# Optimization experiments

Measured on AMD Instinct MI355X. Metric: run time of the kernel, lower is better.

Reference implementation:

```python
import jax, jax.numpy as jnp
import numpy as np

N = 20000
E = 320000
IN_DIM = 128
HID = 64
HEADS = 8
OUT_DIM = 128
NEG_SLOPE = 0.2  # PyG GATConv default leaky_relu slope


def _glorot(key, shape):
    fan_in = shape[0] if len(shape) > 1 else shape[-1]
    return jax.random.normal(key, shape, dtype=jnp.float32) / jnp.sqrt(jnp.float32(fan_in))


def setup_inputs() -> dict:
    key = jax.random.key(0)
    ks = jax.random.split(key, 16)
    x = jax.random.normal(ks[0], (N, IN_DIM), dtype=jnp.float32)
    edge_index = jax.random.randint(ks[1], (2, E), 0, N, dtype=jnp.int32)
    HC = HEADS * HID
    return {
        "x": x,
        "edge_index": edge_index,
        # layer 1: in -> heads*hid (concat)
        "W1": _glorot(ks[2], (IN_DIM, HC)),
        "a_src1": _glorot(ks[3], (HEADS, HID)),
        "a_dst1": _glorot(ks[4], (HEADS, HID)),
        "b1": jnp.zeros((HC,), jnp.float32),
        # layer 2: heads*hid -> heads*hid (concat)
        "W2": _glorot(ks[5], (HC, HC)),
        "a_src2": _glorot(ks[6], (HEADS, HID)),
        "a_dst2": _glorot(ks[7], (HEADS, HID)),
        "b2": jnp.zeros((HC,), jnp.float32),
        # layer 3: heads*hid -> out, heads=1, concat=False
        "W3": _glorot(ks[8], (HC, OUT_DIM)),
        "a_src3": _glorot(ks[9], (1, OUT_DIM)),
        "a_dst3": _glorot(ks[10], (1, OUT_DIM)),
        "b3": jnp.zeros((OUT_DIM,), jnp.float32),
    }


def _gat_layer(x, src, dst, W, a_src, a_dst, b, heads, concat):
    # x: [N, F_in] -> h: [N, H, C]
    n = x.shape[0]
    h = (x @ W).reshape(n, heads, -1)
    # per-node attention half-logits: [N, H]
    al_src = jnp.sum(h * a_src[None], axis=-1)
    al_dst = jnp.sum(h * a_dst[None], axis=-1)
    # per-edge logits with leaky relu: [E, H]
    e = jax.nn.leaky_relu(al_src[src] + al_dst[dst], NEG_SLOPE)
    # segment softmax over incoming edges of each dst node
    emax = jax.ops.segment_max(e, dst, num_segments=n)
    ex = jnp.exp(e - emax[dst])
    den = jax.ops.segment_sum(ex, dst, num_segments=n)
    alpha = ex / (den[dst] + 1e-16)
    # weighted scatter-aggregate of source features: [E, H, C] -> [N, H, C]
    out = jax.ops.segment_sum(h[src] * alpha[:, :, None], dst, num_segments=n)
    out = out.reshape(n, -1) if concat else out.mean(axis=1)
    return out + b


def reference(x, edge_index, W1, a_src1, a_dst1, b1, W2, a_src2, a_dst2, b2,
              W3, a_src3, a_dst3, b3):
    # PyG GATConv adds self-loops by default
    loops = jnp.arange(N, dtype=edge_index.dtype)
    src = jnp.concatenate([edge_index[0], loops])
    dst = jnp.concatenate([edge_index[1], loops])
    # eval mode: dropout is identity
    h = _gat_layer(x, src, dst, W1, a_src1, a_dst1, b1, HEADS, True)
    h = jax.nn.elu(h)
    h = _gat_layer(h, src, dst, W2, a_src2, a_dst2, b2, HEADS, True)
    h = jax.nn.elu(h)
    out = _gat_layer(h, src, dst, W3, a_src3, a_dst3, b3, 1, False)
    return out
```

## Files before the change

kernel.cpp:

```cpp
#include <hip/hip_runtime.h>
#include <math.h>

#define NN 20000
#define EE 320000
#define ETOT 340000
#define NHEADS 8
#define HID 64
#define HCV 512
#define IND 128
#define OUTD 128
#define NEG_SLOPE 0.2f

typedef __attribute__((ext_vector_type(8))) _Float16 half8;
typedef __attribute__((ext_vector_type(4))) float floatx4;

__device__ __forceinline__ void cvt_one(const float* W, _Float16* T, int idx, int K, int N) {
    int k = idx / N, n = idx - k * N;
    T[(size_t)n * K + k] = (_Float16)W[idx];
}

#define S1 (IND * HCV)
#define S2 (HCV * HCV)
#define S3 (HCV * OUTD)
#define STOT (S1 + S2 + S3)
#define XTOT (NN * IND)
__global__ void prep_kernel(const float* __restrict__ W1, const float* __restrict__ W2,
                            const float* __restrict__ W3, const float* __restrict__ x,
                            _Float16* __restrict__ T1, _Float16* __restrict__ T2,
                            _Float16* __restrict__ T3, _Float16* __restrict__ xh,
                            int* __restrict__ cnt) {
    int idx = blockIdx.x * blockDim.x + threadIdx.x;
    if (idx < S1) cvt_one(W1, T1, idx, IND, HCV);
    else if (idx < S1 + S2) cvt_one(W2, T2, idx - S1, HCV, HCV);
    else if (idx < STOT) cvt_one(W3, T3, idx - S1 - S2, HCV, OUTD);
    else if (idx < STOT + NN) cnt[idx - STOT] = 0;
    else if (idx < STOT + NN + XTOT) {
        int j = idx - STOT - NN;
        xh[j] = (_Float16)x[j];
    }
}


__global__ void count_kernel(const int* __restrict__ ei, int* __restrict__ cnt) {
    int i = blockIdx.x * blockDim.x + threadIdx.x;
    if (i >= ETOT) return;
    int v = (i < EE) ? ei[EE + i] : (i - EE);
    atomicAdd(&cnt[v], 1);
}

#define SCH 20
__global__ __launch_bounds__(1024) void scan_kernel(const int* __restrict__ cnt,
                                                    int* __restrict__ row_ptr,
                                                    int* __restrict__ cursor) {
    __shared__ int wtot[16];
    __shared__ int woff[16];
    int t = threadIdx.x;
    int lane = t & 63;
    int wid = t >> 6;
    int base = t * SCH;
    int vals[SCH];
    int s = 0;
    #pragma unroll
    for (int i = 0; i < SCH; i++) {
        int idx = base + i;
        int v = (idx < NN) ? cnt[idx] : 0;
        vals[i] = v;
        s += v;
    }
    int incl = s;
    #pragma unroll
    for (int off = 1; off < 64; off <<= 1) {
        int u = __shfl_up(incl, off);
        if (lane >= off) incl += u;
    }
    int excl = incl - s;
    if (lane == 63) wtot[wid] = incl;
    __syncthreads();
    if (t == 0) {
        int run = 0;
        #pragma unroll
        for (int j = 0; j < 16; j++) { woff[j] = run; run += wtot[j]; }
        row_ptr[NN] = run;
    }
    __syncthreads();
    int run = woff[wid] + excl;
    #pragma unroll
    for (int i = 0; i < SCH; i++) {
        int idx = base + i;
        if (idx < NN) { row_ptr[idx] = run; cursor[idx] = run; run += vals[i]; }
    }
}

__global__ void fill_kernel(const int* __restrict__ ei, int* __restrict__ cursor,
                            int* __restrict__ csr_src) {
    int i = blockIdx.x * blockDim.x + threadIdx.x;
    if (i >= ETOT) return;
    int u, v;
    if (i < EE) { u = ei[i]; v = ei[EE + i]; }
    else        { u = i - EE; v = i - EE; }
    int pos = atomicAdd(&cursor[v], 1);
    csr_src[pos] = u;
}

#define LDK 40
__global__ __launch_bounds__(512) void gemm_al(const _Float16* __restrict__ A,
                                               const _Float16* __restrict__ Bt,
                                               _Float16* __restrict__ C16,
                                               const float* __restrict__ a_src,
                                               const float* __restrict__ a_dst,
                                               float* __restrict__ als2,
                                               float* __restrict__ ald2,
                                               int M, int K) {
    __shared__ _Float16 sA[128 * LDK];
    __shared__ _Float16 sB[128 * LDK];
    __shared__ float psum_s[4][128];
    __shared__ float psum_d[4][128];
    int tid = threadIdx.x;
    int lane = tid & 63;
    int wid = tid >> 6;
    int wv_m = wid >> 2;
    int wv_n = wid & 3;
    int m0 = blockIdx.x * 128, n0 = blockIdx.y * 128;
    int quad = lane >> 4;
    int l15 = lane & 15;
    int arow = tid >> 2;
    int ac4 = tid & 3;

    floatx4 acc[4][2] = {};

    for (int k0 = 0; k0 < K; k0 += 32) {
        {
            int gm = m0 + arow;
            int4 va;
            if (gm < M) va = *(const int4*)&A[(size_t)gm * K + k0 + ac4 * 8];
            else        va = make_int4(0, 0, 0, 0);
            *(int4*)&sA[arow * LDK + ac4 * 8] = va;
            int gn = n0 + arow;
            int4 vb = *(const int4*)&Bt[(size_t)gn * K + k0 + ac4 * 8];
            *(int4*)&sB[arow * LDK + ac4 * 8] = vb;
        }
        __syncthreads();
        half8 a[4], b[2];
        #pragma unroll
        for (int i = 0; i < 4; i++)
            a[i] = *(const half8*)&sA[(wv_m * 64 + i * 16 + l15) * LDK + quad * 8];
        #pragma unroll
        for (int j = 0; j < 2; j++)
            b[j] = *(const half8*)&sB[(wv_n * 32 + j * 16 + l15) * LDK + quad * 8];
        #pragma unroll
        for (int i = 0; i < 4; i++)
            #pragma unroll
            for (int j = 0; j < 2; j++)
                acc[i][j] = __builtin_amdgcn_mfma_f32_16x16x32_f16(a[i], b[j], acc[i][j], 0, 0, 0);
        __syncthreads();
    }
    #pragma unroll
    for (int i = 0; i < 4; i++) {
        #pragma unroll
        for (int r = 0; r < 4; r++) {
            int gm = m0 + wv_m * 64 + i * 16 + quad * 4 + r;
            if (gm < M) {
                #pragma unroll
                for (int j = 0; j < 2; j++)
                    C16[(size_t)gm * HCV + n0 + wv_n * 32 + j * 16 + l15] = (_Float16)acc[i][j][r];
            }
        }
    }
    int h0 = n0 >> 6;
    int hh = h0 + (wv_n >> 1);
    float as_v[2], ad_v[2];
    #pragma unroll
    for (int j = 0; j < 2; j++) {
        int dim = (wv_n * 32 + j * 16 + l15) & 63;
        as_v[j] = a_src[hh * HID + dim];
        ad_v[j] = a_dst[hh * HID + dim];
    }
    #pragma unroll
    for (int i = 0; i < 4; i++) {
        #pragma unroll
        for (int r = 0; r < 4; r++) {
            float ps = acc[i][0][r] * as_v[0] + acc[i][1][r] * as_v[1];
            float pd = acc[i][0][r] * ad_v[0] + acc[i][1][r] * ad_v[1];
            #pragma unroll
            for (int off = 1; off <= 8; off <<= 1) {
                ps += __shfl_xor(ps, off);
                pd += __shfl_xor(pd, off);
            }
            if (l15 == 0) {
                int row = wv_m * 64 + i * 16 + quad * 4 + r;
                psum_s[wv_n][row] = ps;
                psum_d[wv_n][row] = pd;
            }
        }
    }
    __syncthreads();
    if (tid < 128) {
        int gm = m0 + tid;
        if (gm < M) {
            als2[(size_t)h0 * NN + gm]       = psum_s[0][tid] + psum_s[1][tid];
            als2[(size_t)(h0 + 1) * NN + gm] = psum_s[2][tid] + psum_s[3][tid];
            ald2[(size_t)h0 * NN + gm]       = psum_d[0][tid] + psum_d[1][tid];
            ald2[(size_t)(h0 + 1) * NN + gm] = psum_d[2][tid] + psum_d[3][tid];
        }
    }
}

__global__ __launch_bounds__(256) void gemm3(const _Float16* __restrict__ A,
                                             const _Float16* __restrict__ Bt,
                                             _Float16* __restrict__ C16,
                                             const float* __restrict__ a_src,
                                             const float* __restrict__ a_dst,
                                             float* __restrict__ als,
                                             float* __restrict__ ald,
                                             int M, int K) {
    __shared__ _Float16 sA[64 * LDK];
    __shared__ _Float16 sB[128 * LDK];
    __shared__ float psum_s[4][64];
    __shared__ float psum_d[4][64];
    int tid = threadIdx.x;
    int lane = tid & 63;
    int wv = tid >> 6;
    int m0 = blockIdx.x * 64;
    int quad = lane >> 4;
    int l15 = lane & 15;
    int arow = tid >> 2;
    int ac4 = tid & 3;

    floatx4 acc[4][2] = {};

    for (int k0 = 0; k0 < K; k0 += 32) {
        {
            int gm = m0 + arow;
            int4 va;
            if (gm < M && arow < 64) va = *(const int4*)&A[(size_t)gm * K + k0 + ac4 * 8];
            else                     va = make_int4(0, 0, 0, 0);
            if (arow < 64) *(int4*)&sA[arow * LDK + ac4 * 8] = va;
            #pragma unroll
            for (int r = 0; r < 2; r++) {
                int gn = arow + r * 64;
                int4 vb = *(const int4*)&Bt[(size_t)gn * K + k0 + ac4 * 8];
                *(int4*)&sB[(arow + r * 64) * LDK + ac4 * 8] = vb;
            }
        }
        __syncthreads();
        half8 a[4], b[2];
        #pragma unroll
        for (int i = 0; i < 4; i++)
            a[i] = *(const half8*)&sA[(i * 16 + l15) * LDK + quad * 8];
        #pragma unroll
        for (int j = 0; j < 2; j++)
            b[j] = *(const half8*)&sB[(wv * 32 + j * 16 + l15) * LDK + quad * 8];
        #pragma unroll
        for (int i = 0; i < 4; i++)
            #pragma unroll
            for (int j = 0; j < 2; j++)
                acc[i][j] = __builtin_amdgcn_mfma_f32_16x16x32_f16(a[i], b[j], acc[i][j], 0, 0, 0);
        __syncthreads();
    }
    #pragma unroll
    for (int i = 0; i < 4; i++) {
        #pragma unroll
        for (int r = 0; r < 4; r++) {
            int gm = m0 + i * 16 + quad * 4 + r;
            if (gm < M) {
                #pragma unroll
                for (int j = 0; j < 2; j++)
                    C16[(size_t)gm * OUTD + wv * 32 + j * 16 + l15] = (_Float16)acc[i][j][r];
            }
        }
    }
    float as_v[2], ad_v[2];
    #pragma unroll
    for (int j = 0; j < 2; j++) {
        as_v[j] = a_src[wv * 32 + j * 16 + l15];
        ad_v[j] = a_dst[wv * 32 + j * 16 + l15];
    }
    #pragma unroll
    for (int i = 0; i < 4; i++) {
        #pragma unroll
        for (int r = 0; r < 4; r++) {
            float ps = acc[i][0][r] * as_v[0] + acc[i][1][r] * as_v[1];
            float pd = acc[i][0][r] * ad_v[0] + acc[i][1][r] * ad_v[1];
            #pragma unroll
            for (int off = 1; off <= 8; off <<= 1) {
                ps += __shfl_xor(ps, off);
                pd += __shfl_xor(pd, off);
            }
            if (l15 == 0) {
                int row = i * 16 + quad * 4 + r;
                psum_s[wv][row] = ps;
                psum_d[wv][row] = pd;
            }
        }
    }
    __syncthreads();
    if (tid < 64) {
        int gm = m0 + tid;
        if (gm < M) {
            als[gm] = psum_s[0][tid] + psum_s[1][tid] + psum_s[2][tid] + psum_s[3][tid];
            ald[gm] = psum_d[0][tid] + psum_d[1][tid] + psum_d[2][tid] + psum_d[3][tid];
        }
    }
}

__global__ __launch_bounds__(256) void gather_kernel(const _Float16* __restrict__ h,
                                                     const int* __restrict__ row_ptr,
                                                     const int* __restrict__ csr_src,
                                                     const float* __restrict__ als2,
                                                     const float* __restrict__ ald2,
                                                     const float* __restrict__ bias,
                                                     _Float16* __restrict__ gout) {
    int tid = threadIdx.x;
    int lane = tid & 63;
    int wid = tid >> 6;
    int bid = blockIdx.x;
    int hd = bid & 7;
    int sub = lane >> 3;
    int dl = lane & 7;
    int v = (bid >> 3) * 32 + wid * 8 + sub;
    if (v >= NN) return;
    const float* asl = als2 + (size_t)hd * NN;
    float adst = ald2[(size_t)hd * NN + v];
    int s0 = row_ptr[v], s1 = row_ptr[v + 1];
    const _Float16* hh = h + hd * HID + dl * 8;
    float acc[8] = {};
    float l = 0.f;
    int j = s0;
    for (; j + 4 <= s1; j += 4) {
        int u[4]; float p[4]; half8 xv[4];
        #pragma unroll
        for (int e = 0; e < 4; e++) u[e] = csr_src[j + e];
        #pragma unroll
        for (int e = 0; e < 4; e++) xv[e] = *(const half8*)&hh[(size_t)u[e] * HCV];
        #pragma unroll
        for (int e = 0; e < 4; e++) {
            float t = asl[u[e]] + adst;
            t = (t > 0.f) ? t : NEG_SLOPE * t;
            p[e] = __expf(fminf(t, 80.f));
        }
        #pragma unroll
        for (int e = 0; e < 4; e++) {
            l += p[e];
            #pragma unroll
            for (int k = 0; k < 8; k++)
                acc[k] = fmaf(p[e], (float)xv[e][k], acc[k]);
        }
    }
    for (; j < s1; j++) {
        int u0 = csr_src[j];
        half8 x0 = *(const half8*)&hh[(size_t)u0 * HCV];
        float t0 = asl[u0] + adst;
        t0 = (t0 > 0.f) ? t0 : NEG_SLOPE * t0;
        float p0 = __expf(fminf(t0, 80.f));
        l += p0;
        #pragma unroll
        for (int k = 0; k < 8; k++)
            acc[k] = fmaf(p0, (float)x0[k], acc[k]);
    }
    float inv = 1.f / (l + 1e-16f);
    half8 hv;
    #pragma unroll
    for (int k = 0; k < 8; k++) {
        float o = fmaf(acc[k], inv, bias[hd * HID + dl * 8 + k]);
        o = (o > 0.f) ? o : (__expf(o) - 1.f);
        hv[k] = (_Float16)o;
    }
    half8* dst = (half8*)&gout[(size_t)v * HCV + hd * HID + dl * 8];
    __builtin_nontemporal_store(hv, dst);
}

__global__ __launch_bounds__(256) void gather3_kernel(const _Float16* __restrict__ h,
                                                      const int* __restrict__ row_ptr,
                                                      const int* __restrict__ csr_src,
                                                      const float* __restrict__ als,
                                                      const float* __restrict__ ald,
                                                      const float* __restrict__ bias,
                                                      float* __restrict__ out) {
    int tid = threadIdx.x;
    int lane = tid & 63;
    int wid = tid >> 6;
    int bid = blockIdx.x;
    int dh = bid & 1;
    int sub = lane >> 3;
    int dl = lane & 7;
    int v = (bid >> 1) * 32 + wid * 8 + sub;
    if (v >= NN) return;
    float adst = ald[v];
    int s0 = row_ptr[v], s1 = row_ptr[v + 1];
    const _Float16* hh = h + dh * 64 + dl * 8;
    float m = -INFINITY;
    for (int j = s0; j < s1; j++) {
        int u = csr_src[j];
        float t = als[u] + adst;
        t = (t > 0.f) ? t : NEG_SLOPE * t;
        m = fmaxf(m, t);
    }
    float acc[8] = {};
    float l = 0.f;
    int j = s0;
    for (; j + 2 <= s1; j += 2) {
        int u0 = csr_src[j], u1 = csr_src[j + 1];
        float t0 = als[u0] + adst;
        float t1 = als[u1] + adst;
        t0 = (t0 > 0.f) ? t0 : NEG_SLOPE * t0;
        t1 = (t1 > 0.f) ? t1 : NEG_SLOPE * t1;
        float p0 = __expf(t0 - m);
        float p1 = __expf(t1 - m);
        half8 x0 = *(const half8*)&hh[(size_t)u0 * OUTD];
        half8 x1 = *(const half8*)&hh[(size_t)u1 * OUTD];
        l += p0 + p1;
        #pragma unroll
        for (int k = 0; k < 8; k++) {
            acc[k] = fmaf(p0, (float)x0[k], acc[k]);
            acc[k] = fmaf(p1, (float)x1[k], acc[k]);
        }
    }
    if (j < s1) {
        int u0 = csr_src[j];
        float t0 = als[u0] + adst;
        t0 = (t0 > 0.f) ? t0 : NEG_SLOPE * t0;
        float p0 = __expf(t0 - m);
        half8 x0 = *(const half8*)&hh[(size_t)u0 * OUTD];
        l += p0;
        #pragma unroll
        for (int k = 0; k < 8; k++)
            acc[k] = fmaf(p0, (float)x0[k], acc[k]);
    }
    float inv = 1.f / (l + 1e-16f);
    float4 o0, o1;
    o0.x = fmaf(acc[0], inv, bias[dh * 64 + dl * 8 + 0]);
    o0.y = fmaf(acc[1], inv, bias[dh * 64 + dl * 8 + 1]);
    o0.z = fmaf(acc[2], inv, bias[dh * 64 + dl * 8 + 2]);
    o0.w = fmaf(acc[3], inv, bias[dh * 64 + dl * 8 + 3]);
    o1.x = fmaf(acc[4], inv, bias[dh * 64 + dl * 8 + 4]);
    o1.y = fmaf(acc[5], inv, bias[dh * 64 + dl * 8 + 5]);
    o1.z = fmaf(acc[6], inv, bias[dh * 64 + dl * 8 + 6]);
    o1.w = fmaf(acc[7], inv, bias[dh * 64 + dl * 8 + 7]);
    size_t base = (size_t)v * OUTD + dh * 64 + dl * 8;
    *(float4*)&out[base] = o0;
    *(float4*)&out[base + 4] = o1;
}


extern "C" void kernel_launch(void* const* d_in, const int* in_sizes, int n_in,
                              void* d_out, int out_size, void* d_ws, size_t ws_size,
                              hipStream_t stream) {
    const float* x     = (const float*)d_in[0];
    const int*   ei    = (const int*)d_in[1];
    const float* W1    = (const float*)d_in[2];
    const float* as1   = (const float*)d_in[3];
    const float* ad1   = (const float*)d_in[4];
    const float* b1    = (const float*)d_in[5];
    const float* W2    = (const float*)d_in[6];
    const float* as2   = (const float*)d_in[7];
    const float* ad2   = (const float*)d_in[8];
    const float* b2    = (const float*)d_in[9];
    const float* W3    = (const float*)d_in[10];
    const float* as3   = (const float*)d_in[11];
    const float* ad3   = (const float*)d_in[12];
    const float* b3    = (const float*)d_in[13];
    float* out = (float*)d_out;

    size_t off = 0;
    auto carve = [&](size_t bytes) {
        void* p = (char*)d_ws + off;
        off += (bytes + 255) & ~(size_t)255;
        return p;
    };
    int* row_ptr   = (int*)carve((NN + 1) * sizeof(int));
    int* cursor    = (int*)carve(NN * sizeof(int));
    int* csr_src   = (int*)carve(ETOT * sizeof(int));
    _Float16* xh   = (_Float16*)carve((size_t)NN * IND * sizeof(_Float16));
    _Float16* h1   = (_Float16*)carve((size_t)NN * HCV * sizeof(_Float16));
    _Float16* gact = (_Float16*)carve((size_t)NN * HCV * sizeof(_Float16));
    _Float16* hf16 = (_Float16*)carve((size_t)NN * HCV * sizeof(_Float16));
    _Float16* h3   = (_Float16*)carve((size_t)NN * OUTD * sizeof(_Float16));
    float* als     = (float*)carve((size_t)NN * NHEADS * sizeof(float));
    float* ald     = (float*)carve((size_t)NN * NHEADS * sizeof(float));
    _Float16* W1T  = (_Float16*)carve((size_t)S1 * sizeof(_Float16));
    _Float16* W2T  = (_Float16*)carve((size_t)S2 * sizeof(_Float16));
    _Float16* W3T  = (_Float16*)carve((size_t)S3 * sizeof(_Float16));
    _Float16* gact2 = h1;
    (void)ws_size; (void)n_in; (void)in_sizes; (void)out_size;

    dim3 blk(256);

    int prep_n = STOT + NN + XTOT;
    prep_kernel<<<(prep_n + 255) / 256, blk, 0, stream>>>(W1, W2, W3, x,
        W1T, W2T, W3T, xh, cursor);

    count_kernel<<<(ETOT + 255) / 256, blk, 0, stream>>>(ei, cursor);
    scan_kernel<<<1, 1024, 0, stream>>>(cursor, row_ptr, cursor);
    fill_kernel<<<(ETOT + 255) / 256, blk, 0, stream>>>(ei, cursor, csr_src);

    int mt64 = (NN + 63) / 64;
    int mt128 = (NN + 127) / 128;
    int nb = (NN + 31) / 32;

    gemm_al<<<dim3(mt128, HCV / 128), dim3(512), 0, stream>>>(xh, W1T, h1, as1, ad1, als, ald, NN, IND);
    gather_kernel<<<dim3(nb * 8), blk, 0, stream>>>(h1, row_ptr, csr_src, als, ald, b1, gact);

    gemm_al<<<dim3(mt128, HCV / 128), dim3(512), 0, stream>>>(gact, W2T, hf16, as2, ad2, als, ald, NN, HCV);
    gather_kernel<<<dim3(nb * 8), blk, 0, stream>>>(hf16, row_ptr, csr_src, als, ald, b2, gact2);

    gemm3<<<dim3(mt64, 1), blk, 0, stream>>>(gact2, W3T, h3, as3, ad3, als, ald, NN, HCV);
    gather3_kernel<<<dim3(nb * 2), blk, 0, stream>>>(h3, row_ptr, csr_src, als, ald, b3, out);
}
```

Measured before the change: 312.5 us.

## Split edge lists across two lane groups, tile weight transpose, use exp2

The gather kernels now split each destination node's edge range between two 8-lane groups and combine the partial sums and normalisers with a lane shuffle. This doubles the parallelism per node and shortens the serial edge loop. The layer-3 max pass is spread over 16 lanes with a shuffle reduction. The prep kernel replaces the strided per-element weight transpose with shared-memory 32x32 tiles and a float4 vectorised x conversion. The attention vectors are pre-scaled by log2(e) so exp2f can replace expf. The costs are more blocks, cross-lane shuffles, and half the lanes idle during the output epilogue.

```diff
diff --git a/kernel.cpp b/kernel.cpp
--- a/kernel.cpp
+++ b/kernel.cpp
@@ -10,33 +10,63 @@
 #define IND 128
 #define OUTD 128
 #define NEG_SLOPE 0.2f
+#define LOG2E 1.4426950408889634f
 
 typedef __attribute__((ext_vector_type(8))) _Float16 half8;
+typedef __attribute__((ext_vector_type(4))) _Float16 half4;
 typedef __attribute__((ext_vector_type(4))) float floatx4;
-
-__device__ __forceinline__ void cvt_one(const float* W, _Float16* T, int idx, int K, int N) {
-    int k = idx / N, n = idx - k * N;
-    T[(size_t)n * K + k] = (_Float16)W[idx];
-}
 
 #define S1 (IND * HCV)
 #define S2 (HCV * HCV)
 #define S3 (HCV * OUTD)
-#define STOT (S1 + S2 + S3)
 #define XTOT (NN * IND)
-__global__ void prep_kernel(const float* __restrict__ W1, const float* __restrict__ W2,
-                            const float* __restrict__ W3, const float* __restrict__ x,
-                            _Float16* __restrict__ T1, _Float16* __restrict__ T2,
-                            _Float16* __restrict__ T3, _Float16* __restrict__ xh,
-                            int* __restrict__ cnt) {
-    int idx = blockIdx.x * blockDim.x + threadIdx.x;
-    if (idx < S1) cvt_one(W1, T1, idx, IND, HCV);
-    else if (idx < S1 + S2) cvt_one(W2, T2, idx - S1, HCV, HCV);
-    else if (idx < STOT) cvt_one(W3, T3, idx - S1 - S2, HCV, OUTD);
-    else if (idx < STOT + NN) cnt[idx - STOT] = 0;
-    else if (idx < STOT + NN + XTOT) {
-        int j = idx - STOT - NN;
-        xh[j] = (_Float16)x[j];
+
+#define NT1 64
+#define NT2 320
+#define NT_TOT 384
+#define XB 2500
+__global__ __launch_bounds__(256) void prep_kernel(const float* __restrict__ W1,
+                                                   const float* __restrict__ W2,
+                                                   const float* __restrict__ W3,
+                                                   const float* __restrict__ x,
+                                                   _Float16* __restrict__ T1,
+                                                   _Float16* __restrict__ T2,
+                                                   _Float16* __restrict__ T3,
+                                                   _Float16* __restrict__ xh,
+                                                   int* __restrict__ cnt) {
+    int b = blockIdx.x;
+    int tid = threadIdx.x;
+    if (b < NT_TOT) {
+        __shared__ _Float16 tile[32][34];
+        const float* W; _Float16* T; int K, N, tb;
+        if (b < NT1)      { W = W1; T = T1; K = IND; N = HCV;  tb = b; }
+        else if (b < NT2) { W = W2; T = T2; K = HCV; N = HCV;  tb = b - NT1; }
+        else              { W = W3; T = T3; K = HCV; N = OUTD; tb = b - NT2; }
+        int ntn = N >> 5;
+        int k0 = (tb / ntn) * 32, n0 = (tb % ntn) * 32;
+        int tx = tid & 31, ty0 = tid >> 5;
+        #pragma unroll
+        for (int i = 0; i < 4; i++) {
+            int ty = ty0 + 8 * i;
+            tile[ty][tx] = (_Float16)W[(size_t)(k0 + ty) * N + n0 + tx];
+        }
+        __syncthreads();
+        #pragma unroll
+        for (int i = 0; i < 4; i++) {
+            int ty = ty0 + 8 * i;
+            T[(size_t)(n0 + ty) * K + k0 + tx] = tile[tx][ty];
+        }
+    } else if (b < NT_TOT + XB) {
+        int idx = (b - NT_TOT) * 256 + tid;
+        int j = idx * 4;
+        float4 v = *(const float4*)&x[j];
+        half4 o;
+        o[0] = (_Float16)v.x; o[1] = (_Float16)v.y;
+        o[2] = (_Float16)v.z; o[3] = (_Float16)v.w;
+        *(half4*)&xh[j] = o;
+    } else {
+        int idx = (b - NT_TOT - XB) * 256 + tid;
+        if (idx < NN) cnt[idx] = 0;
     }
 }
 
@@ -172,8 +202,8 @@
     #pragma unroll
     for (int j = 0; j < 2; j++) {
         int dim = (wv_n * 32 + j * 16 + l15) & 63;
-        as_v[j] = a_src[hh * HID + dim];
-        ad_v[j] = a_dst[hh * HID + dim];
+        as_v[j] = a_src[hh * HID + dim] * LOG2E;
+        ad_v[j] = a_dst[hh * HID + dim] * LOG2E;
     }
     #pragma unroll
     for (int i = 0; i < 4; i++) {
@@ -272,8 +302,8 @@
     float as_v[2], ad_v[2];
     #pragma unroll
     for (int j = 0; j < 2; j++) {
-        as_v[j] = a_src[wv * 32 + j * 16 + l15];
-        ad_v[j] = a_dst[wv * 32 + j * 16 + l15];
+        as_v[j] = a_src[wv * 32 + j * 16 + l15] * LOG2E;
+        ad_v[j] = a_dst[wv * 32 + j * 16 + l15] * LOG2E;
     }
     #pragma unroll
     for (int i = 0; i < 4; i++) {
@@ -315,18 +345,22 @@
     int wid = tid >> 6;
     int bid = blockIdx.x;
     int hd = bid & 7;
-    int sub = lane >> 3;
     int dl = lane & 7;
-    int v = (bid >> 3) * 32 + wid * 8 + sub;
+    int es = (lane >> 3) & 1;
+    int sub = lane >> 4;
+    int v = (bid >> 3) * 16 + wid * 4 + sub;
     if (v >= NN) return;
     const float* asl = als2 + (size_t)hd * NN;
     float adst = ald2[(size_t)hd * NN + v];
     int s0 = row_ptr[v], s1 = row_ptr[v + 1];
+    int mid = (s0 + s1 + 1) >> 1;
+    int jb = es ? mid : s0;
+    int je = es ? s1 : mid;
     const _Float16* hh = h + hd * HID + dl * 8;
     float acc[8] = {};
     float l = 0.f;
-    int j = s0;
-    for (; j + 4 <= s1; j += 4) {
+    int j = jb;
+    for (; j + 4 <= je; j += 4) {
         int u[4]; float p[4]; half8 xv[4];
         #pragma unroll
         for (int e = 0; e < 4; e++) u[e] = csr_src[j + e];
@@ -336,7 +370,7 @@
         for (int e = 0; e < 4; e++) {
             float t = asl[u[e]] + adst;
             t = (t > 0.f) ? t : NEG_SLOPE * t;
-            p[e] = __expf(fminf(t, 80.f));
+            p[e] = exp2f(fminf(t, 115.f));
         }
         #pragma unroll
         for (int e = 0; e < 4; e++) {
@@ -346,27 +380,33 @@
                 acc[k] = fmaf(p[e], (float)xv[e][k], acc[k]);
         }
     }
-    for (; j < s1; j++) {
+    for (; j < je; j++) {
         int u0 = csr_src[j];
         half8 x0 = *(const half8*)&hh[(size_t)u0 * HCV];
         float t0 = asl[u0] + adst;
         t0 = (t0 > 0.f) ? t0 : NEG_SLOPE * t0;
-        float p0 = __expf(fminf(t0, 80.f));
+        float p0 = exp2f(fminf(t0, 115.f));
         l += p0;
         #pragma unroll
         for (int k = 0; k < 8; k++)
             acc[k] = fmaf(p0, (float)x0[k], acc[k]);
     }
-    float inv = 1.f / (l + 1e-16f);
-    half8 hv;
-    #pragma unroll
-    for (int k = 0; k < 8; k++) {
-        float o = fmaf(acc[k], inv, bias[hd * HID + dl * 8 + k]);
-        o = (o > 0.f) ? o : (__expf(o) - 1.f);
-        hv[k] = (_Float16)o;
-    }
-    half8* dst = (half8*)&gout[(size_t)v * HCV + hd * HID + dl * 8];
-    __builtin_nontemporal_store(hv, dst);
+    l += __shfl_xor(l, 8);
+    #pragma unroll
+    for (int k = 0; k < 8; k++)
+        acc[k] += __shfl_xor(acc[k], 8);
+    if (es == 0) {
+        float inv = 1.f / (l + 1e-16f);
+        half8 hv;
+        #pragma unroll
+        for (int k = 0; k < 8; k++) {
+            float o = fmaf(acc[k], inv, bias[hd * HID + dl * 8 + k]);
+            o = (o > 0.f) ? o : (__expf(o) - 1.f);
+            hv[k] = (_Float16)o;
+        }
+        half8* dst = (half8*)&gout[(size_t)v * HCV + hd * HID + dl * 8];
+        __builtin_nontemporal_store(hv, dst);
+    }
 }
 
 __global__ __launch_bounds__(256) void gather3_kernel(const _Float16* __restrict__ h,
@@ -381,31 +421,39 @@
     int wid = tid >> 6;
     int bid = blockIdx.x;
     int dh = bid & 1;
-    int sub = lane >> 3;
     int dl = lane & 7;
-    int v = (bid >> 1) * 32 + wid * 8 + sub;
+    int es = (lane >> 3) & 1;
+    int sub = lane >> 4;
+    int l16 = lane & 15;
+    int v = (bid >> 1) * 16 + wid * 4 + sub;
     if (v >= NN) return;
     float adst = ald[v];
     int s0 = row_ptr[v], s1 = row_ptr[v + 1];
-    const _Float16* hh = h + dh * 64 + dl * 8;
     float m = -INFINITY;
-    for (int j = s0; j < s1; j++) {
+    for (int j = s0 + l16; j < s1; j += 16) {
         int u = csr_src[j];
         float t = als[u] + adst;
         t = (t > 0.f) ? t : NEG_SLOPE * t;
         m = fmaxf(m, t);
     }
+    #pragma unroll
+    for (int off = 1; off <= 8; off <<= 1)
+        m = fmaxf(m, __shfl_xor(m, off));
+    int mid = (s0 + s1 + 1) >> 1;
+    int jb = es ? mid : s0;
+    int je = es ? s1 : mid;
+    const _Float16* hh = h + dh * 64 + dl * 8;
     float acc[8] = {};
     float l = 0.f;
-    int j = s0;
-    for (; j + 2 <= s1; j += 2) {
+    int j = jb;
+    for (; j + 2 <= je; j += 2) {
         int u0 = csr_src[j], u1 = csr_src[j + 1];
         float t0 = als[u0] + adst;
         float t1 = als[u1] + adst;
         t0 = (t0 > 0.f) ? t0 : NEG_SLOPE * t0;
         t1 = (t1 > 0.f) ? t1 : NEG_SLOPE * t1;
-        float p0 = __expf(t0 - m);
-        float p1 = __expf(t1 - m);
+        float p0 = exp2f(t0 - m);
+        float p1 = exp2f(t1 - m);
         half8 x0 = *(const half8*)&hh[(size_t)u0 * OUTD];
         half8 x1 = *(const half8*)&hh[(size_t)u1 * OUTD];
         l += p0 + p1;
@@ -415,30 +463,36 @@
             acc[k] = fmaf(p1, (float)x1[k], acc[k]);
         }
     }
-    if (j < s1) {
+    if (j < je) {
         int u0 = csr_src[j];
         float t0 = als[u0] + adst;
         t0 = (t0 > 0.f) ? t0 : NEG_SLOPE * t0;
-        float p0 = __expf(t0 - m);
+        float p0 = exp2f(t0 - m);
         half8 x0 = *(const half8*)&hh[(size_t)u0 * OUTD];
         l += p0;
         #pragma unroll
         for (int k = 0; k < 8; k++)
             acc[k] = fmaf(p0, (float)x0[k], acc[k]);
     }
-    float inv = 1.f / (l + 1e-16f);
-    float4 o0, o1;
-    o0.x = fmaf(acc[0], inv, bias[dh * 64 + dl * 8 + 0]);
-    o0.y = fmaf(acc[1], inv, bias[dh * 64 + dl * 8 + 1]);
-    o0.z = fmaf(acc[2], inv, bias[dh * 64 + dl * 8 + 2]);
-    o0.w = fmaf(acc[3], inv, bias[dh * 64 + dl * 8 + 3]);
-    o1.x = fmaf(acc[4], inv, bias[dh * 64 + dl * 8 + 4]);
-    o1.y = fmaf(acc[5], inv, bias[dh * 64 + dl * 8 + 5]);
-    o1.z = fmaf(acc[6], inv, bias[dh * 64 + dl * 8 + 6]);
-    o1.w = fmaf(acc[7], inv, bias[dh * 64 + dl * 8 + 7]);
-    size_t base = (size_t)v * OUTD + dh * 64 + dl * 8;
-    *(float4*)&out[base] = o0;
-    *(float4*)&out[base + 4] = o1;
+    l += __shfl_xor(l, 8);
+    #pragma unroll
+    for (int k = 0; k < 8; k++)
+        acc[k] += __shfl_xor(acc[k], 8);
+    if (es == 0) {
+        float inv = 1.f / (l + 1e-16f);
+        float4 o0, o1;
+        o0.x = fmaf(acc[0], inv, bias[dh * 64 + dl * 8 + 0]);
+        o0.y = fmaf(acc[1], inv, bias[dh * 64 + dl * 8 + 1]);
+        o0.z = fmaf(acc[2], inv, bias[dh * 64 + dl * 8 + 2]);
+        o0.w = fmaf(acc[3], inv, bias[dh * 64 + dl * 8 + 3]);
+        o1.x = fmaf(acc[4], inv, bias[dh * 64 + dl * 8 + 4]);
+        o1.y = fmaf(acc[5], inv, bias[dh * 64 + dl * 8 + 5]);
+        o1.z = fmaf(acc[6], inv, bias[dh * 64 + dl * 8 + 6]);
+        o1.w = fmaf(acc[7], inv, bias[dh * 64 + dl * 8 + 7]);
+        size_t base = (size_t)v * OUTD + dh * 64 + dl * 8;
+        *(float4*)&out[base] = o0;
+        *(float4*)&out[base + 4] = o1;
+    }
 }
 
 
@@ -485,9 +539,8 @@
 
     dim3 blk(256);
 
-    int prep_n = STOT + NN + XTOT;
-    prep_kernel<<<(prep_n + 255) / 256, blk, 0, stream>>>(W1, W2, W3, x,
-        W1T, W2T, W3T, xh, cursor);
+    int prep_blocks = NT_TOT + XB + (NN + 255) / 256;
+    prep_kernel<<<prep_blocks, blk, 0, stream>>>(W1, W2, W3, x, W1T, W2T, W3T, xh, cursor);
 
     count_kernel<<<(ETOT + 255) / 256, blk, 0, stream>>>(ei, cursor);
     scan_kernel<<<1, 1024, 0, stream>>>(cursor, row_ptr, cursor);
@@ -495,14 +548,14 @@
 
     int mt64 = (NN + 63) / 64;
     int mt128 = (NN + 127) / 128;
-    int nb = (NN + 31) / 32;
+    int nb4 = (NN + 15) / 16;
 
     gemm_al<<<dim3(mt128, HCV / 128), dim3(512), 0, stream>>>(xh, W1T, h1, as1, ad1, als, ald, NN, IND);
-    gather_kernel<<<dim3(nb * 8), blk, 0, stream>>>(h1, row_ptr, csr_src, als, ald, b1, gact);
+    gather_kernel<<<dim3(nb4 * 8), blk, 0, stream>>>(h1, row_ptr, csr_src, als, ald, b1, gact);
 
     gemm_al<<<dim3(mt128, HCV / 128), dim3(512), 0, stream>>>(gact, W2T, hf16, as2, ad2, als, ald, NN, HCV);
-    gather_kernel<<<dim3(nb * 8), blk, 0, stream>>>(hf16, row_ptr, csr_src, als, ald, b2, gact2);
+    gather_kernel<<<dim3(nb4 * 8), blk, 0, stream>>>(hf16, row_ptr, csr_src, als, ald, b2, gact2);
 
     gemm3<<<dim3(mt64, 1), blk, 0, stream>>>(gact2, W3T, h3, as3, ad3, als, ald, NN, HCV);
-    gather3_kernel<<<dim3(nb * 2), blk, 0, stream>>>(h3, row_ptr, csr_src, als, ald, b3, out);
-}
+    gather3_kernel<<<dim3(nb4 * 2), blk, 0, stream>>>(h3, row_ptr, csr_src, als, ald, b3, out);
+}
```

Result: no change. 310.1 us (-0.8%).
